# Kernel optimization log

Hardware: AMD Instinct MI355X
Metric: run time of the kernel (lower is better)

The kernel has to match this reference:

```python
import jax, jax.numpy as jnp
import numpy as np

B = 1024        # interactions per batch (graphs per side)
DIM = 64        # args.dim
HID = 64        # args.hidd_dim == args.word_dim
L = 2           # args.num_layers
NREL = 4        # relation types
N_USERS, N_ITEMS, N_WORDS = 100000, 50000, 50000
N = 131072      # total nodes per batched graph (per side)
E = 524288      # total edges per batched graph (per side)
D_FM = (L + 1) * DIM * 2  # 384


def setup_inputs() -> dict:
    key = jax.random.key(0)
    ks = iter(jax.random.split(key, 64))
    nrm = lambda shape, s=0.05: jax.random.normal(next(ks), shape, jnp.float32) * s
    ri = lambda shape, hi: jax.random.randint(next(ks), shape, 0, hi)
    # deterministic sorted graph-membership vector: equal-size graphs, no empty segments
    batch = (jnp.arange(N) * B) // N
    return dict(
        uid=ri((B,), N_USERS), iid=ri((B,), N_ITEMS),
        u_nodes=ri((N,), N_WORDS), i_nodes=ri((N,), N_WORDS),
        u_edge_index=ri((2, E), N), i_edge_index=ri((2, E), N),
        u_edge_type=ri((E,), NREL), i_edge_type=ri((E,), NREL),
        u_batch=batch, i_batch=batch,
        user_emb=nrm((N_USERS, DIM)), item_emb=nrm((N_ITEMS, DIM)), word_emb=nrm((N_WORDS, HID)),
        trans_u_W=nrm((L, DIM, HID)), trans_u_b=jnp.zeros((L, HID)),
        trans_i_W=nrm((L, DIM, HID)), trans_i_b=jnp.zeros((L, HID)),
        trans_w_W=nrm((L, HID, DIM)), trans_w_b=jnp.zeros((L, DIM)),
        inter_u_W=nrm((DIM, DIM)), inter_u_b=jnp.zeros((DIM,)),
        inter_i_W=nrm((DIM, DIM)), inter_i_b=jnp.zeros((DIM,)),
        conv_u_W=nrm((L, HID, HID)), conv_u_b=jnp.zeros((L, HID)),
        conv_u_att=nrm((L, 3, HID)), conv_u_rel=nrm((L, NREL, HID)),
        conv_i_W=nrm((L, HID, HID)), conv_i_b=jnp.zeros((L, HID)),
        conv_i_att=nrm((L, 3, HID)), conv_i_rel=nrm((L, NREL, HID)),
        pool_W=nrm((HID, HID)),
        fm_w=nrm((D_FM,)), fm_V=nrm((D_FM, D_FM)),
        fm_bias_u=jnp.zeros((N_USERS,)), fm_bias_i=jnp.zeros((N_ITEMS,)), fm_bias=jnp.zeros((1,)),
    )


def _gat(x, ei, et, W, b, att, rel):
    """Relational GAT conv: attention over incoming edges with relation-type term."""
    n = x.shape[0]
    h = x @ W + b                         # [n, HID]
    src, dst = ei[0], ei[1]
    e = jax.nn.leaky_relu(h[src] @ att[0] + h[dst] @ att[1] + rel[et] @ att[2], 0.2)  # [E]
    emax = jax.ops.segment_max(e, dst, num_segments=n)
    emax = jnp.where(jnp.isfinite(emax), emax, 0.0)   # guard nodes with no in-edges
    ex = jnp.exp(e - emax[dst])
    den = jax.ops.segment_sum(ex, dst, num_segments=n)
    alpha = ex / (den[dst] + 1e-16)
    return jax.nn.relu(jax.ops.segment_sum(alpha[:, None] * h[src], dst, num_segments=n))


def _conv_pool(ui_em, x, ei, et, batch, Ws, bs, atts, rels, tw_W, tw_b, pool_W, nb):
    """L stages of GAT conv -> query-conditioned soft pooling gate -> global max pool."""
    inv_sqrt_d = 1.0 / np.sqrt(HID).astype(np.float32)
    outs = []
    for i in range(L):
        x = _gat(x, ei, et, Ws[i], bs[i], atts[i], rels[i])
        q = ui_em[i]                                          # [B, HID] per-graph query
        score = jax.nn.sigmoid(jnp.sum((x @ pool_W) * q[batch], -1) * inv_sqrt_d)  # [N]
        x = x * score[:, None]
        pooled = jax.ops.segment_max(x, batch, num_segments=nb)  # gmp -> [B, HID]
        outs.append(jax.nn.relu(pooled @ tw_W[i] + tw_b[i]))     # trans_w -> [B, DIM]
    return jnp.concatenate(outs, -1)                             # [B, L*DIM]


def reference(uid, iid, u_nodes, i_nodes, u_edge_index, i_edge_index,
              u_edge_type, i_edge_type, u_batch, i_batch,
              user_emb, item_emb, word_emb,
              trans_u_W, trans_u_b, trans_i_W, trans_i_b, trans_w_W, trans_w_b,
              inter_u_W, inter_u_b, inter_i_W, inter_i_b,
              conv_u_W, conv_u_b, conv_u_att, conv_u_rel,
              conv_i_W, conv_i_b, conv_i_att, conv_i_rel,
              pool_W, fm_w, fm_V, fm_bias_u, fm_bias_i, fm_bias):
    u_e = user_emb[uid]                                        # [B, DIM]
    i_e = item_emb[iid]
    u_em = [jax.nn.relu(u_e @ trans_u_W[i] + trans_u_b[i]) for i in range(L)]
    i_em = [jax.nn.relu(i_e @ trans_i_W[i] + trans_i_b[i]) for i in range(L)]
    u_pool = _conv_pool(u_em, word_emb[u_nodes], u_edge_index, u_edge_type, u_batch,
                        conv_u_W, conv_u_b, conv_u_att, conv_u_rel,
                        trans_w_W, trans_w_b, pool_W, B)
    i_pool = _conv_pool(i_em, word_emb[i_nodes], i_edge_index, i_edge_type, i_batch,
                        conv_i_W, conv_i_b, conv_i_att, conv_i_rel,
                        trans_w_W, trans_w_b, pool_W, B)
    user_rep = jax.nn.relu(u_e @ inter_u_W + inter_u_b)
    item_rep = jax.nn.relu(i_e @ inter_i_W + inter_i_b)
    x = jnp.concatenate([user_rep, u_pool, item_rep, i_pool], -1)   # [B, D_FM]
    # FM layer (degree-2 interaction with full V matrix, as in source)
    linear = x @ fm_w                                               # [B]
    xv = x @ fm_V                                                   # [B, D_FM]
    mlp = 0.5 * jnp.sum(xv * xv - (x * x) @ (fm_V * fm_V), -1)
    return linear + mlp + fm_bias_u[uid] + fm_bias_i[iid] + fm_bias[0]
```

## Files before the change

kernel.cpp:

```cpp
#include <hip/hip_runtime.h>
#include <hip/hip_bf16.h>

#define NN 131072
#define NE 524288
#define NB 1024

typedef __attribute__((ext_vector_type(8))) short short8;
typedef __attribute__((ext_vector_type(4))) float f32x4;

__device__ __forceinline__ float wsum(float v){
#pragma unroll
  for (int o = 32; o > 0; o >>= 1) v += __shfl_xor(v, o, 64);
  return v;
}
__device__ __forceinline__ short f2bs(float f){
  __hip_bfloat16 t = __float2bfloat16(f);
  union { __hip_bfloat16 b; short s; } u; u.b = t; return u.s;
}
__device__ __forceinline__ float bs2f(short s){
  return __uint_as_float(((unsigned)(unsigned short)s) << 16);
}
__device__ __forceinline__ float ulo2f(unsigned v){ return __uint_as_float(v << 16); }
__device__ __forceinline__ float uhi2f(unsigned v){ return __uint_as_float(v & 0xFFFF0000u); }
__device__ __forceinline__ unsigned fpack(float x, float y){
  return (unsigned)(unsigned short)f2bs(x) | ((unsigned)(unsigned short)f2bs(y) << 16);
}

__global__ void k_mega(int wconvB,
                       const int* __restrict__ u_ei, const int* __restrict__ i_ei,
                       int* __restrict__ cnt, int* __restrict__ loff,
                       const float* __restrict__ wemb, unsigned* __restrict__ wtab,
                       int n32,
                       const float* __restrict__ cuW, const float* __restrict__ ciW,
                       const float* __restrict__ pW,
                       const float* __restrict__ cub, const float* __restrict__ cib,
                       const float* __restrict__ uatt, const float* __restrict__ iatt,
                       const float* __restrict__ urel, const float* __restrict__ irel,
                       short8* __restrict__ frag, float* __restrict__ waA,
                       float* __restrict__ ba, float* __restrict__ rtab,
                       const int* __restrict__ uid, const int* __restrict__ iid,
                       const float* __restrict__ uemb, const float* __restrict__ iemb,
                       const float* __restrict__ uiW, const float* __restrict__ uib,
                       const float* __restrict__ iiW, const float* __restrict__ iib,
                       const float* __restrict__ utW, const float* __restrict__ utb,
                       const float* __restrict__ itW, const float* __restrict__ itb,
                       float* __restrict__ xfm, float* __restrict__ q){
  const int histB = 2 * NE / 256;
  int blk = blockIdx.x, tid = threadIdx.x;
  if (blk < histB){
    int ee = blk * 256 + tid;
    int side = ee >= NE;
    int e = ee - side * NE;
    const int* ei = side ? i_ei : u_ei;
    int dst = ei[NE + e] + side * NN;
    int p = atomicAdd(&cnt[dst << 2], 1);
    loff[ee] = p;
  } else if (blk < histB + 10){
    int b2 = blk - histB;
    int mat = b2 >> 1;
    const float* W = mat < 2 ? cuW + mat * 4096 : (mat < 4 ? ciW + (mat - 2) * 4096 : pW);
    int g = (b2 & 1) * 256 + tid;
    int lane = g & 63, rest = g >> 6;
    int hh = rest & 1, t = rest >> 1;
    int m = lane & 15, qq = lane >> 4;
    short8 v;
#pragma unroll
    for (int j = 0; j < 8; j++)
      v[j] = f2bs(W[(hh * 32 + qq * 8 + j) * 64 + (t * 16 + m)]);
    frag[mat * 512 + g] = v;
  } else if (blk < histB + 12){
    int side = blk - histB - 10;
    const float* W    = side ? ciW : cuW;
    const float* bias = side ? cib : cub;
    const float* att  = side ? iatt : uatt;
    const float* rel  = side ? irel : urel;
    int l = tid >> 7, a = (tid >> 6) & 1, kk = tid & 63;
    float s = 0.f;
    for (int c = 0; c < 64; c++) s += W[l * 4096 + kk * 64 + c] * att[l * 192 + a * 64 + c];
    waA[((side * 2 + l) * 2 + a) * 64 + kk] = s;
    if (tid < 4){
      int l2 = tid >> 1, a2 = tid & 1;
      float sb = 0.f;
      for (int c = 0; c < 64; c++) sb += bias[l2 * 64 + c] * att[l2 * 192 + a2 * 64 + c];
      ba[(side * 2 + l2) * 2 + a2] = sb;
    }
    if (tid >= 4 && tid < 12){
      int id = tid - 4, l2 = id >> 2, tt = id & 3;
      float sr = 0.f;
      for (int c = 0; c < 64; c++) sr += rel[l2 * 256 + tt * 64 + c] * att[l2 * 192 + 128 + c];
      rtab[(side * 2 + l2) * 4 + tt] = sr;
    }
  } else if (blk < histB + 12 + wconvB){
    int id = (blk - histB - 12) * 256 + tid;
    if (id < n32){
      const float2* src = (const float2*)wemb;
      float2 v = src[id];
      wtab[id] = fpack(v.x, v.y);
    }
  } else {
    int lane = tid & 63, w = tid >> 6;
    int b = (blk - histB - 12 - wconvB) * 4 + w;
    int side = b >= NB;
    int lb = b - side * NB;
    const int* ids = side ? iid : uid;
    const float* emb = side ? iemb : uemb;
    const float* interW = side ? iiW : uiW;
    const float* interB = side ? iib : uib;
    const float* transW = side ? itW : utW;
    const float* transB = side ? itb : utb;
    int repOff = side ? 192 : 0;
    float xe = emb[(long)ids[lb] * 64 + lane];
    float o = interB[lane];
#pragma unroll
    for (int k = 0; k < 64; k++) o += __shfl(xe, k, 64) * interW[k * 64 + lane];
    xfm[lb * 384 + repOff + lane] = fmaxf(o, 0.f);
    for (int l = 0; l < 2; l++){
      float t = transB[l * 64 + lane];
#pragma unroll
      for (int k = 0; k < 64; k++) t += __shfl(xe, k, 64) * transW[l * 4096 + k * 64 + lane];
      q[((size_t)(side * 2 + l) * NB + lb) * 64 + lane] = fmaxf(t, 0.f);
    }
  }
}

__global__ void k_scan1(const int* __restrict__ cnt, int* __restrict__ rowptr,
                        int* __restrict__ bsum){
  __shared__ int sh[256];
  int i = blockIdx.x * 256 + threadIdx.x;
  int v = cnt[i << 2];
  sh[threadIdx.x] = v; __syncthreads();
  for (int off = 1; off < 256; off <<= 1){
    int t = (threadIdx.x >= off) ? sh[threadIdx.x - off] : 0;
    __syncthreads();
    sh[threadIdx.x] += t;
    __syncthreads();
  }
  int incl = sh[threadIdx.x];
  rowptr[i] = incl - v;
  if (threadIdx.x == 255) bsum[blockIdx.x] = incl;
}

__global__ void k_scan2(int* __restrict__ bsum){
  __shared__ int sh[1024];
  int v = bsum[threadIdx.x];
  sh[threadIdx.x] = v; __syncthreads();
  for (int off = 1; off < 1024; off <<= 1){
    int t = (threadIdx.x >= off) ? sh[threadIdx.x - off] : 0;
    __syncthreads();
    sh[threadIdx.x] += t;
    __syncthreads();
  }
  bsum[threadIdx.x] = sh[threadIdx.x] - v;
}

__global__ void k_scw(const int* __restrict__ u_ei, const int* __restrict__ i_ei,
                      const int* __restrict__ u_et, const int* __restrict__ i_et,
                      const int* __restrict__ rowptr, const int* __restrict__ bsum,
                      const int* __restrict__ loff, int* __restrict__ pedge,
                      int* __restrict__ rowfin,
                      const short* __restrict__ wtab, int nwords, int wgB,
                      const float* __restrict__ waA, const float* __restrict__ ba,
                      float* __restrict__ wa0, float* __restrict__ wa1){
  const int scatB = 2 * NE / 256;
  int blk = blockIdx.x, tid = threadIdx.x;
  if (blk < scatB){
    int ee = blk * 256 + tid;
    int side = ee >= NE;
    int e = ee - side * NE;
    const int* ei = side ? i_ei : u_ei;
    const int* et = side ? i_et : u_et;
    int dst = ei[NE + e] + side * NN;
    int src = ei[e] + side * NN;
    int p = rowptr[dst] + bsum[dst >> 8] + loff[ee];
    pedge[p] = src | (et[e] << 18);
  } else if (blk < scatB + wgB){
    int lane = tid & 63, w = tid >> 6;
    int q = lane >> 4, cl = lane & 15;
    int sw0 = ((blk - scatB) * 4 + w) * 8;
    const uint2* wt2 = (const uint2*)wtab;
    for (int it = 0; it < 2; it++){
      int wj = sw0 + it * 4 + q;
      if (wj >= 2 * nwords) continue;
      int side = wj >= nwords;
      int wid = wj - side * nwords;
      const float* A0 = waA + (side * 2 + 0) * 2 * 64;
      const float* A1 = A0 + 64;
      uint2 v = wt2[(long)wid * 16 + cl];
      int d = 4 * cl;
      float p0 = ulo2f(v.x) * A0[d] + uhi2f(v.x) * A0[d + 1] +
                 ulo2f(v.y) * A0[d + 2] + uhi2f(v.y) * A0[d + 3];
      float p1 = ulo2f(v.x) * A1[d] + uhi2f(v.x) * A1[d + 1] +
                 ulo2f(v.y) * A1[d + 2] + uhi2f(v.y) * A1[d + 3];
      p0 += __shfl_xor(p0, 1, 64); p0 += __shfl_xor(p0, 2, 64);
      p0 += __shfl_xor(p0, 4, 64); p0 += __shfl_xor(p0, 8, 64);
      p1 += __shfl_xor(p1, 1, 64); p1 += __shfl_xor(p1, 2, 64);
      p1 += __shfl_xor(p1, 4, 64); p1 += __shfl_xor(p1, 8, 64);
      if (cl == 0){
        wa0[(size_t)side * nwords + wid] = p0 + ba[side * 4 + 0];
        wa1[(size_t)side * nwords + wid] = p1 + ba[side * 4 + 1];
      }
    }
  } else {
    int i = (blk - scatB - wgB) * 256 + tid;
    rowfin[i] = rowptr[i] + bsum[i >> 8];
    if (i == 0) rowfin[2 * NN] = 2 * NE;
  }
}

template<int L>
__device__ __forceinline__ void dev_agg(
    const int* __restrict__ rowptr, const int* __restrict__ pedge,
    const float* __restrict__ a0, const float* __restrict__ a1,
    const float* __restrict__ wa0, const float* __restrict__ wa1,
    const int* __restrict__ u_nodes, const int* __restrict__ i_nodes, int nwords,
    const float* __restrict__ rtab, const short* __restrict__ rows,
    unsigned* __restrict__ xo32){
  int lane = threadIdx.x & 63, w = threadIdx.x >> 6;
  int nb = (blockIdx.x * 4 + w) * 8;
  int side = nb >= NN;
  const float* rt = rtab + (side * 2 + L) * 4;
  float rt0 = rt[0], rt1 = rt[1], rt2 = rt[2], rt3 = rt[3];
  const int* nodesS = side ? i_nodes : u_nodes;
  const float* wa0S = wa0 + (size_t)side * nwords;
  const float* wa1S = wa1 + (size_t)side * nwords;
  int q = lane >> 4, cl = lane & 15;
  int rp = (lane < 9) ? rowptr[nb + lane] : 0;
  float a1v = 0.f;
  if (L == 0){
    if (lane < 8) a1v = wa1S[nodesS[nb + lane - side * NN]];
  } else {
    if (lane < 8) a1v = a1[nb + lane];
  }
  int rp0 = __shfl(rp, 0, 64);
  int rp8 = __shfl(rp, 8, 64);
  int tot = min(rp8 - rp0, 64);
  int eidx = rp0 + lane;
  int pe = (lane < tot) ? pedge[eidx] : 0;
  int psrc = pe & 0x3FFFF;
  int prow; float pa0 = 0.f;
  if (L == 0){
    int wid = (lane < tot) ? nodesS[psrc - side * NN] : 0;
    prow = wid;
    if (lane < tot) pa0 = wa0S[wid];
  } else {
    prow = psrc;
    if (lane < tot) pa0 = a0[psrc];
  }
  int kn = 0;
#pragma unroll
  for (int t = 1; t < 8; t++)
    kn += (eidx >= __shfl(rp, t, 64)) ? 1 : 0;
  float a1n = __shfl(a1v, kn, 64);
  int pet = (pe >> 18) & 3;
  float rr = (pet & 2) ? ((pet & 1) ? rt3 : rt2) : ((pet & 1) ? rt1 : rt0);
  float vv = pa0 + a1n + rr;
  vv = (vv > 0.f) ? vv : 0.2f * vv;
  float pex = (lane < tot) ? __expf(vv) : 0.f;
  const uint2* h2 = (const uint2*)rows;
#pragma unroll
  for (int k = 0; k < 8; k++){
    int r0 = __shfl(rp, k, 64), r1 = __shfl(rp, k + 1, 64);
    float a1k = __shfl(a1v, k, 64);
    float ax0 = 0.f, ay0 = 0.f, ax1 = 0.f, ay1 = 0.f, den = 0.f;
    for (int j = r0; j < r1; j += 4){
      int e = j + q;
      bool ok = e < r1;
      int idx = e - rp0;
      int idxc = min(idx, 63);
      int s = __shfl(prow, idxc, 64);
      float ex = __shfl(pex, idxc, 64);
      if (idx >= 64 && ok){
        int pe2 = pedge[e];
        int s2 = pe2 & 0x3FFFF;
        int et2 = (pe2 >> 18) & 3;
        float r2 = (et2 & 2) ? ((et2 & 1) ? rt3 : rt2) : ((et2 & 1) ? rt1 : rt0);
        float av;
        if (L == 0){ int wid = nodesS[s2 - side * NN]; av = wa0S[wid]; s = wid; }
        else       { av = a0[s2]; s = s2; }
        float v2 = av + a1k + r2;
        v2 = (v2 > 0.f) ? v2 : 0.2f * v2;
        ex = __expf(v2);
      }
      if (ok){
        uint2 v = h2[(long)s * 16 + cl];
        ax0 += ex * ulo2f(v.x); ay0 += ex * uhi2f(v.x);
        ax1 += ex * ulo2f(v.y); ay1 += ex * uhi2f(v.y);
        den += ex;
      }
    }
    ax0 += __shfl_xor(ax0, 16, 64); ax0 += __shfl_xor(ax0, 32, 64);
    ay0 += __shfl_xor(ay0, 16, 64); ay0 += __shfl_xor(ay0, 32, 64);
    ax1 += __shfl_xor(ax1, 16, 64); ax1 += __shfl_xor(ax1, 32, 64);
    ay1 += __shfl_xor(ay1, 16, 64); ay1 += __shfl_xor(ay1, 32, 64);
    den += __shfl_xor(den, 16, 64); den += __shfl_xor(den, 32, 64);
    float inv = 1.f / (den + 1e-16f);
    if (q == 0){
      uint2 o;
      o.x = fpack(ax0 * inv, ay0 * inv);
      o.y = fpack(ax1 * inv, ay1 * inv);
      ((uint2*)xo32)[(long)(nb + k) * 16 + cl] = o;
    }
  }
}

__global__ __launch_bounds__(256) void k_agg0(
    const int* __restrict__ rowptr, const int* __restrict__ pedge,
    const float* __restrict__ wa0, const float* __restrict__ wa1,
    const int* __restrict__ u_nodes, const int* __restrict__ i_nodes, int nwords,
    const float* __restrict__ rtab, const short* __restrict__ wtab,
    unsigned* __restrict__ xo32){
  dev_agg<0>(rowptr, pedge, nullptr, nullptr, wa0, wa1, u_nodes, i_nodes, nwords,
             rtab, wtab, xo32);
}

__global__ __launch_bounds__(256) void k_agg1(
    const int* __restrict__ rowptr, const int* __restrict__ pedge,
    const float* __restrict__ a0, const float* __restrict__ a1,
    const float* __restrict__ rtab, const short* __restrict__ x,
    unsigned* __restrict__ xo32){
  dev_agg<1>(rowptr, pedge, a0, a1, nullptr, nullptr, nullptr, nullptr, 0,
             rtab, x, xo32);
}

__global__ __launch_bounds__(256) void k_gp(
    int l, const short* __restrict__ xagg, const short8* __restrict__ frag,
    const float* __restrict__ cub, const float* __restrict__ cib,
    const float* __restrict__ waA_all, const float* __restrict__ ba_all,
    const float* __restrict__ qbuf, const float* __restrict__ twW_all,
    const float* __restrict__ twb_all, float* __restrict__ xfm,
    short* __restrict__ xnext, float* __restrict__ a0, float* __restrict__ a1){
  __shared__ short xt[128 * 72];
  __shared__ float gates[128];
  __shared__ float red[4][64];
  int b = blockIdx.x;
  int side = b >= NB;
  int g = b - side * NB;
  long base = (long)side * NN + (long)g * 128;
  int tid = threadIdx.x, lane = tid & 63, w = tid >> 6;
  int m = lane & 15, q = lane >> 4;
  const short8* wfrag = frag + (side * 2 + l) * 512;
  const float* bias = (side ? cib : cub) + l * 64;
  short8 Bf[4][2];
#pragma unroll
  for (int t = 0; t < 4; t++)
#pragma unroll
    for (int hh = 0; hh < 2; hh++)
      Bf[t][hh] = wfrag[(t * 2 + hh) * 64 + lane];
  float bs[4];
#pragma unroll
  for (int t = 0; t < 4; t++) bs[t] = bias[t * 16 + m];
  f32x4 accA[2][4];
#pragma unroll
  for (int rb = 0; rb < 2; rb++){
    long n0 = base + w * 32 + rb * 16;
    const short8* xr = (const short8*)(xagg + (n0 + m) * 64);
    short8 A0 = xr[q];
    short8 A1 = xr[q + 4];
#pragma unroll
    for (int t = 0; t < 4; t++){
      f32x4 acc = (f32x4){bs[t], bs[t], bs[t], bs[t]};
      acc = __builtin_amdgcn_mfma_f32_16x16x32_bf16(A0, Bf[t][0], acc, 0, 0, 0);
      acc = __builtin_amdgcn_mfma_f32_16x16x32_bf16(A1, Bf[t][1], acc, 0, 0, 0);
#pragma unroll
      for (int r = 0; r < 4; r++) acc[r] = fmaxf(acc[r], 0.f);
      accA[rb][t] = acc;
#pragma unroll
      for (int r = 0; r < 4; r++)
        xt[(w * 32 + rb * 16 + q * 4 + r) * 72 + t * 16 + m] = f2bs(acc[r]);
    }
  }
  __syncthreads();
  const short8* pfrag = frag + 4 * 512;
  const float* qv_ = qbuf + ((size_t)(side * 2 + l) * NB + g) * 64;
  short8 Pf[4][2];
#pragma unroll
  for (int t = 0; t < 4; t++)
#pragma unroll
    for (int hh = 0; hh < 2; hh++)
      Pf[t][hh] = pfrag[(t * 2 + hh) * 64 + lane];
  float qv[4];
#pragma unroll
  for (int t = 0; t < 4; t++) qv[t] = qv_[t * 16 + m];
#pragma unroll
  for (int rb = 0; rb < 2; rb++){
    int rowb = w * 32 + rb * 16;
    short8 A0 = *(const short8*)(xt + (rowb + m) * 72 + q * 8);
    short8 A1 = *(const short8*)(xt + (rowb + m) * 72 + 32 + q * 8);
    f32x4 accp[4];
#pragma unroll
    for (int t = 0; t < 4; t++){
      accp[t] = (f32x4){0.f, 0.f, 0.f, 0.f};
      accp[t] = __builtin_amdgcn_mfma_f32_16x16x32_bf16(A0, Pf[t][0], accp[t], 0, 0, 0);
      accp[t] = __builtin_amdgcn_mfma_f32_16x16x32_bf16(A1, Pf[t][1], accp[t], 0, 0, 0);
    }
#pragma unroll
    for (int r = 0; r < 4; r++){
      float p = accp[0][r] * qv[0] + accp[1][r] * qv[1] +
                accp[2][r] * qv[2] + accp[3][r] * qv[3];
      p += __shfl_xor(p, 1, 64); p += __shfl_xor(p, 2, 64);
      p += __shfl_xor(p, 4, 64); p += __shfl_xor(p, 8, 64);
      if (m == 0)
        gates[rowb + q * 4 + r] = 1.f / (1.f + __expf(-p * 0.125f));
    }
  }
  __syncthreads();
  const unsigned* xt32 = (const unsigned*)xt;
  int c = lane & 31, half = lane >> 5;
  float mxx = 0.f, mxy = 0.f;
#pragma unroll
  for (int p = 0; p < 16; p++){
    int nn = w * 32 + 2 * p + half;
    unsigned v = xt32[nn * 36 + c];
    float gt = gates[nn];
    mxx = fmaxf(mxx, ulo2f(v) * gt);
    mxy = fmaxf(mxy, uhi2f(v) * gt);
  }
  mxx = fmaxf(mxx, __shfl_xor(mxx, 32, 64));
  mxy = fmaxf(mxy, __shfl_xor(mxy, 32, 64));
  if (half == 0){ red[w][2 * c] = mxx; red[w][2 * c + 1] = mxy; }
  __syncthreads();
  if (tid < 64){
    const float* twW = twW_all + l * 4096;
    const float* twb = twb_all + l * 64;
    int off = (side ? 256 : 64) + l * 64;
    float p = fmaxf(fmaxf(red[0][tid], red[1][tid]), fmaxf(red[2][tid], red[3][tid]));
    float o = twb[tid];
    red[0][tid] = p;
    __syncwarp();
    for (int d = 0; d < 64; d++) o += red[0][d] * twW[d * 64 + tid];
    xfm[g * 384 + off + tid] = fmaxf(o, 0.f);
  }
  if (l == 0){
#pragma unroll
    for (int p = 0; p < 4; p++){
      int row = p * 32 + (tid >> 3);
      int col8 = (tid & 7) * 8;
      float gt = gates[row];
      short8 v = *(const short8*)(xt + row * 72 + col8);
      short8 o;
#pragma unroll
      for (int j = 0; j < 8; j++) o[j] = f2bs(bs2f(v[j]) * gt);
      *(short8*)(xnext + (base + row) * 64 + col8) = o;
    }
    const float* wn0p = waA_all + ((side * 2 + 1) * 2 + 0) * 64;
    const float* wn1p = wn0p + 64;
    float wn0[4], wn1[4];
#pragma unroll
    for (int t = 0; t < 4; t++){ wn0[t] = wn0p[t * 16 + m]; wn1[t] = wn1p[t * 16 + m]; }
    float ban0 = ba_all[(side * 2 + 1) * 2 + 0];
    float ban1 = ba_all[(side * 2 + 1) * 2 + 1];
#pragma unroll
    for (int rb = 0; rb < 2; rb++)
#pragma unroll
      for (int r = 0; r < 4; r++){
        float p0 = accA[rb][0][r] * wn0[0] + accA[rb][1][r] * wn0[1] +
                   accA[rb][2][r] * wn0[2] + accA[rb][3][r] * wn0[3];
        float p1 = accA[rb][0][r] * wn1[0] + accA[rb][1][r] * wn1[1] +
                   accA[rb][2][r] * wn1[2] + accA[rb][3][r] * wn1[3];
        p0 += __shfl_xor(p0, 1, 64); p0 += __shfl_xor(p0, 2, 64);
        p0 += __shfl_xor(p0, 4, 64); p0 += __shfl_xor(p0, 8, 64);
        p1 += __shfl_xor(p1, 1, 64); p1 += __shfl_xor(p1, 2, 64);
        p1 += __shfl_xor(p1, 4, 64); p1 += __shfl_xor(p1, 8, 64);
        if (m == 0){
          int row = w * 32 + rb * 16 + q * 4 + r;
          float gr = gates[row];
          a0[base + row] = p0 * gr + ban0;
          a1[base + row] = p1 * gr + ban1;
        }
      }
  }
}

__global__ __launch_bounds__(384) void k_fm(
    const float* __restrict__ xfm, const float* __restrict__ V,
    const float* __restrict__ fw, const float* __restrict__ bu,
    const float* __restrict__ bi, const float* __restrict__ b0,
    const int* __restrict__ uid, const int* __restrict__ iid,
    float* __restrict__ out){
  __shared__ float xsh[4][384];
  __shared__ float xsq[4][384];
  __shared__ float part[4][384];
  int j = threadIdx.x;
  int g0 = blockIdx.x * 4;
#pragma unroll
  for (int b = 0; b < 4; b++){
    float xv_ = xfm[(g0 + b) * 384 + j];
    xsh[b][j] = xv_;
    xsq[b][j] = xv_ * xv_;
  }
  __syncthreads();
  float xv[4] = {0.f, 0.f, 0.f, 0.f};
  float vv[4] = {0.f, 0.f, 0.f, 0.f};
  for (int k = 0; k < 384; k++){
    float v = V[(size_t)k * 384 + j];
    float v2 = v * v;
#pragma unroll
    for (int b = 0; b < 4; b++){
      xv[b] = fmaf(xsh[b][k], v, xv[b]);
      vv[b] = fmaf(xsq[b][k], v2, vv[b]);
    }
  }
  float fwj = fw[j];
#pragma unroll
  for (int b = 0; b < 4; b++)
    part[b][j] = 0.5f * (xv[b] * xv[b] - vv[b]) + xsh[b][j] * fwj;
  __syncthreads();
  int w = j >> 6, lane = j & 63;
  if (w < 4){
    float s = part[w][lane] + part[w][lane + 64] + part[w][lane + 128] +
              part[w][lane + 192] + part[w][lane + 256] + part[w][lane + 320];
    s = wsum(s);
    if (lane == 0){
      int b = g0 + w;
      out[b] = s + bu[uid[b]] + bi[iid[b]] + b0[0];
    }
  }
}

extern "C" void kernel_launch(void* const* d_in, const int* in_sizes, int n_in,
                              void* d_out, int out_size, void* d_ws, size_t ws_size,
                              hipStream_t stream) {
  const int* uid      = (const int*)d_in[0];
  const int* iid      = (const int*)d_in[1];
  const int* u_nodes  = (const int*)d_in[2];
  const int* i_nodes  = (const int*)d_in[3];
  const int* u_ei     = (const int*)d_in[4];
  const int* i_ei     = (const int*)d_in[5];
  const int* u_et     = (const int*)d_in[6];
  const int* i_et     = (const int*)d_in[7];
  const float* user_emb = (const float*)d_in[10];
  const float* item_emb = (const float*)d_in[11];
  const float* word_emb = (const float*)d_in[12];
  const float* trans_u_W = (const float*)d_in[13];
  const float* trans_u_b = (const float*)d_in[14];
  const float* trans_i_W = (const float*)d_in[15];
  const float* trans_i_b = (const float*)d_in[16];
  const float* trans_w_W = (const float*)d_in[17];
  const float* trans_w_b = (const float*)d_in[18];
  const float* inter_u_W = (const float*)d_in[19];
  const float* inter_u_b = (const float*)d_in[20];
  const float* inter_i_W = (const float*)d_in[21];
  const float* inter_i_b = (const float*)d_in[22];
  const float* conv_u_W  = (const float*)d_in[23];
  const float* conv_u_b  = (const float*)d_in[24];
  const float* conv_u_att= (const float*)d_in[25];
  const float* conv_u_rel= (const float*)d_in[26];
  const float* conv_i_W  = (const float*)d_in[27];
  const float* conv_i_b  = (const float*)d_in[28];
  const float* conv_i_att= (const float*)d_in[29];
  const float* conv_i_rel= (const float*)d_in[30];
  const float* pool_W    = (const float*)d_in[31];
  const float* fm_w      = (const float*)d_in[32];
  const float* fm_V      = (const float*)d_in[33];
  const float* fm_bias_u = (const float*)d_in[34];
  const float* fm_bias_i = (const float*)d_in[35];
  const float* fm_bias   = (const float*)d_in[36];
  float* out = (float*)d_out;
  int n32 = in_sizes[12] / 2;
  int nwords = in_sizes[12] / 64;
  int wconvB = (n32 + 255) / 256;

  char* w = (char*)d_ws;
  short* X0   = (short*)w;          w += (size_t)2 * NN * 64 * 2;
  short* X1   = (short*)w;          w += (size_t)2 * NN * 64 * 2;
  short* wtab = (short*)w;          w += (size_t)in_sizes[12] * 2;
  int* pedge  = (int*)w;            w += (size_t)2 * NE * 4;
  float* a0   = (float*)w;          w += (size_t)2 * NN * 4;
  float* a1   = (float*)w;          w += (size_t)2 * NN * 4;
  float* wa0  = (float*)w;          w += (size_t)2 * nwords * 4;
  float* wa1  = (float*)w;          w += (size_t)2 * nwords * 4;
  int* rowptr = (int*)w;            w += (size_t)2 * NN * 4;
  int* rowfin = (int*)w;            w += (size_t)(2 * NN + 256) * 4;
  int* bsum   = (int*)w;            w += 1024 * 4;
  short8* frag = (short8*)w;        w += (size_t)5 * 512 * 16;
  float* waA  = (float*)w;          w += 2 * 2 * 2 * 64 * 4;
  float* ba   = (float*)w;          w += 64;
  float* rtab = (float*)w;          w += 64;
  float* qbuf = (float*)w;          w += (size_t)4 * NB * 64 * 4;
  float* xfm  = (float*)w;          w += (size_t)NB * 384 * 4;
  int* cnt  = (int*)X1;
  int* loff = (int*)X0;

  hipMemsetAsync(cnt, 0, (size_t)2 * NN * 16, stream);

  int histB = 2 * NE / 256;
  int megaB = histB + 12 + wconvB + 2 * NB / 4;
  k_mega<<<megaB, 256, 0, stream>>>(wconvB, u_ei, i_ei, cnt, loff,
                                    word_emb, (unsigned*)wtab, n32,
                                    conv_u_W, conv_i_W, pool_W, conv_u_b, conv_i_b,
                                    conv_u_att, conv_i_att, conv_u_rel, conv_i_rel,
                                    frag, waA, ba, rtab,
                                    uid, iid, user_emb, item_emb,
                                    inter_u_W, inter_u_b, inter_i_W, inter_i_b,
                                    trans_u_W, trans_u_b, trans_i_W, trans_i_b,
                                    xfm, qbuf);
  k_scan1<<<2 * NN / 256, 256, 0, stream>>>(cnt, rowptr, bsum);
  k_scan2<<<1, 1024, 0, stream>>>(bsum);
  int wgB = (2 * nwords + 31) / 32;
  int scatB = 2 * NE / 256;
  int finB = 2 * NN / 256;
  k_scw<<<scatB + wgB + finB, 256, 0, stream>>>(u_ei, i_ei, u_et, i_et,
                                                rowptr, bsum, loff, pedge, rowfin,
                                                wtab, nwords, wgB, waA, ba, wa0, wa1);

  k_agg0<<<2 * NN / 32, 256, 0, stream>>>(rowfin, pedge, wa0, wa1,
                                          u_nodes, i_nodes, nwords, rtab,
                                          wtab, (unsigned*)X0);
  k_gp  <<<2 * NB, 256, 0, stream>>>(0, X0, frag, conv_u_b, conv_i_b, waA, ba,
                                     qbuf, trans_w_W, trans_w_b, xfm, X1, a0, a1);
  k_agg1<<<2 * NN / 32, 256, 0, stream>>>(rowfin, pedge, a0, a1, rtab,
                                          X1, (unsigned*)X0);
  k_gp  <<<2 * NB, 256, 0, stream>>>(1, X0, frag, conv_u_b, conv_i_b, waA, ba,
                                     qbuf, trans_w_W, trans_w_b, xfm,
                                     nullptr, nullptr, nullptr);

  k_fm<<<NB / 4, 384, 0, stream>>>(xfm, fm_V, fm_w, fm_bias_u, fm_bias_i, fm_bias,
                                   uid, iid, out);
}
```

Baseline: 431.5 us.

## Map one node per 16-lane group in GAT aggregation instead of 8 nodes per wave

Rewrites the edge aggregation so each 16-lane quarter-wave handles one destination node and walks its edges serially. This replaces the previous scheme, where a wave took 8 nodes, prefetched their edge metadata cooperatively and used shuffles plus cross-quarter reductions. The launch grid doubles to match. The new mapping drops the shuffle and reduction overhead and the serial loop over 8 nodes, but each lane now loads pedge, the attention scalar and the exp redundantly per edge, and degree imbalance inside a wave can cause divergence.

After: 438.7 us. No clear change (+1.7%).

```diff
diff --git a/kernel.cpp b/kernel.cpp
--- a/kernel.cpp
+++ b/kernel.cpp
@@ -216,91 +216,43 @@
     const float* __restrict__ rtab, const short* __restrict__ rows,
     unsigned* __restrict__ xo32){
   int lane = threadIdx.x & 63, w = threadIdx.x >> 6;
-  int nb = (blockIdx.x * 4 + w) * 8;
-  int side = nb >= NN;
+  int grp = lane >> 4, cl = lane & 15;
+  int n = (blockIdx.x * 4 + w) * 4 + grp;
+  int side = n >= NN;
   const float* rt = rtab + (side * 2 + L) * 4;
   float rt0 = rt[0], rt1 = rt[1], rt2 = rt[2], rt3 = rt[3];
   const int* nodesS = side ? i_nodes : u_nodes;
   const float* wa0S = wa0 + (size_t)side * nwords;
   const float* wa1S = wa1 + (size_t)side * nwords;
-  int q = lane >> 4, cl = lane & 15;
-  int rp = (lane < 9) ? rowptr[nb + lane] : 0;
-  float a1v = 0.f;
-  if (L == 0){
-    if (lane < 8) a1v = wa1S[nodesS[nb + lane - side * NN]];
-  } else {
-    if (lane < 8) a1v = a1[nb + lane];
-  }
-  int rp0 = __shfl(rp, 0, 64);
-  int rp8 = __shfl(rp, 8, 64);
-  int tot = min(rp8 - rp0, 64);
-  int eidx = rp0 + lane;
-  int pe = (lane < tot) ? pedge[eidx] : 0;
-  int psrc = pe & 0x3FFFF;
-  int prow; float pa0 = 0.f;
-  if (L == 0){
-    int wid = (lane < tot) ? nodesS[psrc - side * NN] : 0;
-    prow = wid;
-    if (lane < tot) pa0 = wa0S[wid];
-  } else {
-    prow = psrc;
-    if (lane < tot) pa0 = a0[psrc];
-  }
-  int kn = 0;
-#pragma unroll
-  for (int t = 1; t < 8; t++)
-    kn += (eidx >= __shfl(rp, t, 64)) ? 1 : 0;
-  float a1n = __shfl(a1v, kn, 64);
-  int pet = (pe >> 18) & 3;
-  float rr = (pet & 2) ? ((pet & 1) ? rt3 : rt2) : ((pet & 1) ? rt1 : rt0);
-  float vv = pa0 + a1n + rr;
-  vv = (vv > 0.f) ? vv : 0.2f * vv;
-  float pex = (lane < tot) ? __expf(vv) : 0.f;
   const uint2* h2 = (const uint2*)rows;
-#pragma unroll
-  for (int k = 0; k < 8; k++){
-    int r0 = __shfl(rp, k, 64), r1 = __shfl(rp, k + 1, 64);
-    float a1k = __shfl(a1v, k, 64);
-    float ax0 = 0.f, ay0 = 0.f, ax1 = 0.f, ay1 = 0.f, den = 0.f;
-    for (int j = r0; j < r1; j += 4){
-      int e = j + q;
-      bool ok = e < r1;
-      int idx = e - rp0;
-      int idxc = min(idx, 63);
-      int s = __shfl(prow, idxc, 64);
-      float ex = __shfl(pex, idxc, 64);
-      if (idx >= 64 && ok){
-        int pe2 = pedge[e];
-        int s2 = pe2 & 0x3FFFF;
-        int et2 = (pe2 >> 18) & 3;
-        float r2 = (et2 & 2) ? ((et2 & 1) ? rt3 : rt2) : ((et2 & 1) ? rt1 : rt0);
-        float av;
-        if (L == 0){ int wid = nodesS[s2 - side * NN]; av = wa0S[wid]; s = wid; }
-        else       { av = a0[s2]; s = s2; }
-        float v2 = av + a1k + r2;
-        v2 = (v2 > 0.f) ? v2 : 0.2f * v2;
-        ex = __expf(v2);
-      }
-      if (ok){
-        uint2 v = h2[(long)s * 16 + cl];
-        ax0 += ex * ulo2f(v.x); ay0 += ex * uhi2f(v.x);
-        ax1 += ex * ulo2f(v.y); ay1 += ex * uhi2f(v.y);
-        den += ex;
-      }
-    }
-    ax0 += __shfl_xor(ax0, 16, 64); ax0 += __shfl_xor(ax0, 32, 64);
-    ay0 += __shfl_xor(ay0, 16, 64); ay0 += __shfl_xor(ay0, 32, 64);
-    ax1 += __shfl_xor(ax1, 16, 64); ax1 += __shfl_xor(ax1, 32, 64);
-    ay1 += __shfl_xor(ay1, 16, 64); ay1 += __shfl_xor(ay1, 32, 64);
-    den += __shfl_xor(den, 16, 64); den += __shfl_xor(den, 32, 64);
-    float inv = 1.f / (den + 1e-16f);
-    if (q == 0){
-      uint2 o;
-      o.x = fpack(ax0 * inv, ay0 * inv);
-      o.y = fpack(ax1 * inv, ay1 * inv);
-      ((uint2*)xo32)[(long)(nb + k) * 16 + cl] = o;
-    }
-  }
+
+  int r0 = rowptr[n], r1 = rowptr[n + 1];
+  float a1n;
+  if (L == 0) a1n = wa1S[nodesS[n - side * NN]];
+  else        a1n = a1[n];
+
+  float ax0 = 0.f, ay0 = 0.f, ax1 = 0.f, ay1 = 0.f, den = 0.f;
+  for (int e = r0; e < r1; ++e){
+    int pe = pedge[e];
+    int s = pe & 0x3FFFF;
+    int et = (pe >> 18) & 3;
+    float rr = (et & 2) ? ((et & 1) ? rt3 : rt2) : ((et & 1) ? rt1 : rt0);
+    float av; long row;
+    if (L == 0){ int wid = nodesS[s - side * NN]; av = wa0S[wid]; row = wid; }
+    else       { av = a0[s]; row = s; }
+    float v = av + a1n + rr;
+    v = (v > 0.f) ? v : 0.2f * v;
+    float ex = __expf(v);
+    uint2 hv = h2[row * 16 + cl];
+    ax0 += ex * ulo2f(hv.x); ay0 += ex * uhi2f(hv.x);
+    ax1 += ex * ulo2f(hv.y); ay1 += ex * uhi2f(hv.y);
+    den += ex;
+  }
+  float inv = 1.f / (den + 1e-16f);
+  uint2 o;
+  o.x = fpack(ax0 * inv, ay0 * inv);
+  o.y = fpack(ax1 * inv, ay1 * inv);
+  ((uint2*)xo32)[(long)n * 16 + cl] = o;
 }
 
 __global__ __launch_bounds__(256) void k_agg0(
@@ -603,12 +555,12 @@
                                                 rowptr, bsum, loff, pedge, rowfin,
                                                 wtab, nwords, wgB, waA, ba, wa0, wa1);
 
-  k_agg0<<<2 * NN / 32, 256, 0, stream>>>(rowfin, pedge, wa0, wa1,
+  k_agg0<<<2 * NN / 16, 256, 0, stream>>>(rowfin, pedge, wa0, wa1,
                                           u_nodes, i_nodes, nwords, rtab,
                                           wtab, (unsigned*)X0);
   k_gp  <<<2 * NB, 256, 0, stream>>>(0, X0, frag, conv_u_b, conv_i_b, waA, ba,
                                      qbuf, trans_w_W, trans_w_b, xfm, X1, a0, a1);
-  k_agg1<<<2 * NN / 32, 256, 0, stream>>>(rowfin, pedge, a0, a1, rtab,
+  k_agg1<<<2 * NN / 16, 256, 0, stream>>>(rowfin, pedge, a0, a1, rtab,
                                           X1, (unsigned*)X0);
   k_gp  <<<2 * NB, 256, 0, stream>>>(1, X0, frag, conv_u_b, conv_i_b, waA, ba,
                                      qbuf, trans_w_W, trans_w_b, xfm,
```
